# Performance work log

Hardware: AMD Instinct MI355X
Metric: run time of the kernel (lower is better)

Reference implementation:

```python
import jax, jax.numpy as jnp
import numpy as np

D1 = 2  # Predictor d1
D2 = 3  # Predictor d2


def setup_inputs() -> dict:
    key = jax.random.key(0)
    ks = jax.random.split(key, 8)
    B, S, W = 256, 16, 32
    V, E, H, C = 30000, 256, 512, 5
    abstracts = jax.random.randint(ks[0], (B, S, W), 0, V, dtype=jnp.int32)
    emb_table = jax.random.normal(ks[1], (V, E), dtype=jnp.float32) * 0.1
    # torch LSTMCell params: weight_ih [4H,E], weight_hh [4H,H], biases [4H]
    sc = 1.0 / np.sqrt(H)
    Wih = jax.random.uniform(ks[2], (4 * H, E), jnp.float32, -sc, sc)
    Whh = jax.random.uniform(ks[3], (4 * H, H), jnp.float32, -sc, sc)
    b_ih = jax.random.uniform(ks[4], (4 * H,), jnp.float32, -sc, sc)
    b_hh = jax.random.uniform(ks[5], (4 * H,), jnp.float32, -sc, sc)
    # Predictor: d1+1 weights [H,C], d2+1 weights [C,C], zero biases [1,C]
    W1 = jax.random.normal(ks[6], (D1 + 1, H, C), dtype=jnp.float32)
    W2 = jax.random.normal(ks[7], (D2 + 1, C, C), dtype=jnp.float32)
    b1 = jnp.zeros((1, C), dtype=jnp.float32)
    b2 = jnp.zeros((1, C), dtype=jnp.float32)
    return {"abstracts": abstracts, "emb_table": emb_table, "Wih": Wih,
            "Whh": Whh, "b_ih": b_ih, "b_hh": b_hh,
            "W1": W1, "b1": b1, "W2": W2, "b2": b2}


def _lstm_scan(x_tbe, Wih, Whh, b_ih, b_hh):
    # x_tbe: [T, B, E] time-major; state carried across ALL timesteps
    T, B, _ = x_tbe.shape
    H = Whh.shape[1]
    bias = b_ih + b_hh

    def step(carry, x):
        h, c = carry
        gates = x @ Wih.T + h @ Whh.T + bias  # [B, 4H]
        i_, f_, g_, o_ = jnp.split(gates, 4, axis=-1)
        c2 = jax.nn.sigmoid(f_) * c + jax.nn.sigmoid(i_) * jnp.tanh(g_)
        h2 = jax.nn.sigmoid(o_) * jnp.tanh(c2)
        return (h2, c2), h2

    init = (jnp.zeros((B, H), x_tbe.dtype), jnp.zeros((B, H), x_tbe.dtype))
    _, hs = jax.lax.scan(step, init, x_tbe)  # [T, B, H]
    return hs


def _predictor(reps, W1, b1, W2, b2):
    # reps: [S, B, H] sentence representations
    S = reps.shape[0]
    C = W1.shape[-1]
    # A[m] = tanh(sum_{k<=min(m,d1)} reps[m-k] @ W1[k] + b1)
    P = jnp.einsum('sbh,khc->ksbc', reps, W1)  # [d1+1, S, B, C]
    A_pre = jnp.zeros(reps.shape[:2] + (C,), reps.dtype)
    for k in range(D1 + 1):
        A_pre = A_pre.at[k:].add(P[k][:S - k])
    A = jnp.tanh(A_pre + b1)  # [S, B, C]
    # main branch (i >= d2): pred_i = logsoftmax(sum_t A[i-d2+t] @ W2[t] + b2)
    Q = jnp.einsum('sbc,tcd->tsbd', A, W2)  # [d2+1, S, B, C]
    M = sum(Q[t][t:S - D2 + t] for t in range(D2 + 1)) + b2  # [S-d2, B, C]
    # fallback (i < d2): logsoftmax(tanh(reps[i] @ W1[0] + b1) @ W2[0] + b2)
    F = jnp.tanh(jnp.einsum('sbh,hc->sbc', reps[:D2], W1[0]) + b1) @ W2[0] + b2
    preds = jnp.concatenate([jax.nn.log_softmax(F, axis=-1),
                             jax.nn.log_softmax(M, axis=-1)], axis=0)
    return preds  # [S, B, C]


def reference(abstracts, emb_table, Wih, Whh, b_ih, b_hh, W1, b1, W2, b2):
    B, S, W = abstracts.shape
    H = Whh.shape[1]
    emb = emb_table[abstracts]                 # [B, S, W, E]
    emb = jnp.transpose(emb, (1, 2, 0, 3))     # [S, W, B, E]
    x = emb.reshape(S * W, B, emb.shape[-1])   # time-major over all words
    hs = _lstm_scan(x, Wih, Whh, b_ih, b_hh)   # [S*W, B, H]
    hs = hs.reshape(S, W, B, H)
    reps = jnp.max(hs, axis=1)                 # max-pool over words -> [S, B, H]
    # dropout is identity in eval mode
    preds = _predictor(reps, W1, b1, W2, b2)   # [S, B, C]
    return jnp.transpose(preds, (1, 2, 0))     # [B, C, S]
```

## Files before the change

kernel.cpp:

```cpp
#include <hip/hip_runtime.h>
#include <cstdint>
#include <cstddef>

typedef float    f32x4  __attribute__((ext_vector_type(4)));
typedef short    s16x8  __attribute__((ext_vector_type(8)));
typedef _Float16 f16x8  __attribute__((ext_vector_type(8)));
typedef uint16_t u16x4  __attribute__((ext_vector_type(4)));

#define D_B 256
#define D_S 16
#define D_W 32
#define D_T 512
#define D_V 30000
#define D_E 256
#define D_H 512
#define D_G 2048
#define D_C 5

constexpr size_t OFF_EG    = 0;
constexpr size_t OFF_EMB   = OFF_EG   + (size_t)D_V * D_G * 2;
constexpr size_t OFF_WIH   = OFF_EMB  + (size_t)D_V * D_E * 2;
constexpr size_t OFF_WHH   = OFF_WIH  + (size_t)D_G * D_E * 2;
constexpr size_t OFF_BIAS  = OFF_WHH  + (size_t)D_G * D_H * 2;
constexpr size_t OFF_HBUF  = OFF_BIAS + (size_t)D_G * 4;
constexpr size_t OFF_FLAGS = OFF_HBUF + (size_t)2 * D_B * D_H * 2;
constexpr size_t OFF_REPS  = OFF_FLAGS + (size_t)256 * 4;
constexpr size_t OFF_A     = OFF_REPS + (size_t)D_S * D_B * D_H * 4;
constexpr size_t OFF_A0    = OFF_A    + (size_t)D_S * D_B * D_C * 4;
constexpr size_t OFF_ABT   = OFF_A0   + (size_t)3 * D_B * D_C * 4;


__device__ __forceinline__ uint16_t f2h(float f) {
    _Float16 h = (_Float16)f;
    return __builtin_bit_cast(uint16_t, h);
}
__device__ __forceinline__ float sigm(float x)  { return 1.0f / (1.0f + __expf(-x)); }
__device__ __forceinline__ float tanh_fast(float x) { return 1.0f - 2.0f / (__expf(2.0f * x) + 1.0f); }

#define VWAIT(N) do { asm volatile("s_waitcnt vmcnt(" #N ")" ::: "memory"); \
                      __builtin_amdgcn_sched_barrier(0); } while (0)
#define SBAR()   __builtin_amdgcn_sched_barrier(0)

__device__ __forceinline__ int load_flag_llc(const int* p) {
    int v;
    asm volatile("global_load_dword %0, %1, off sc0 sc1\n\ts_waitcnt vmcnt(0)"
                 : "=v"(v) : "v"(p) : "memory");
    return v;
}
__device__ __forceinline__ void store_dword_llc(int* p, int v) {
    asm volatile("global_store_dword %0, %1, off sc0 sc1" :: "v"(p), "v"(v) : "memory");
}
__device__ __forceinline__ void store16_llc(void* p, f32x4 v) {
    asm volatile("global_store_dwordx4 %0, %1, off sc0 sc1" :: "v"(p), "v"(v) : "memory");
}
__device__ __forceinline__ void store_h_nowait(uint16_t* p, f16x8 v) {
    asm volatile("global_store_dwordx4 %0, %1, off sc0 sc1" :: "v"(p), "v"(v) : "memory");
}
__device__ __forceinline__ void issue_tok(const int* p, int& v) {
    asm volatile("global_load_dword %0, %1, off" : "=&v"(v) : "v"(p) : "memory");
}
__device__ __forceinline__ void issue_eg(const uint16_t* p, f16x8& a, f16x8& b2,
                                         f16x8& c, f16x8& d) {
    asm volatile(
        "global_load_dwordx4 %0, %4, off\n\t"
        "global_load_dwordx4 %1, %4, off offset:16\n\t"
        "global_load_dwordx4 %2, %4, off offset:32\n\t"
        "global_load_dwordx4 %3, %4, off offset:48"
        : "=&v"(a), "=&v"(b2), "=&v"(c), "=&v"(d)
        : "v"(p) : "memory");
}
__device__ __forceinline__ void issue_h8(const uint16_t* base, f16x8* A) {
    const uint16_t* base2 = base + 2048;
    asm volatile(
        "global_load_dwordx4 %0, %8, off sc0 sc1\n\t"
        "global_load_dwordx4 %1, %8, off offset:1024 sc0 sc1\n\t"
        "global_load_dwordx4 %2, %8, off offset:2048 sc0 sc1\n\t"
        "global_load_dwordx4 %3, %8, off offset:3072 sc0 sc1\n\t"
        "global_load_dwordx4 %4, %9, off sc0 sc1\n\t"
        "global_load_dwordx4 %5, %9, off offset:1024 sc0 sc1\n\t"
        "global_load_dwordx4 %6, %9, off offset:2048 sc0 sc1\n\t"
        "global_load_dwordx4 %7, %9, off offset:3072 sc0 sc1"
        : "=&v"(A[0]), "=&v"(A[1]), "=&v"(A[2]), "=&v"(A[3]),
          "=&v"(A[4]), "=&v"(A[5]), "=&v"(A[6]), "=&v"(A[7])
        : "v"(base), "v"(base2) : "memory");
}

__global__ __launch_bounds__(256) void prep_kernel(
    const int* __restrict__ abstracts,
    const float* __restrict__ emb, const float* __restrict__ Wih,
    const float* __restrict__ Whh, const float* __restrict__ bih,
    const float* __restrict__ bhh,
    uint16_t* __restrict__ embB, uint16_t* __restrict__ WihP,
    uint16_t* __restrict__ WhhP, float* __restrict__ biasP,
    uint16_t* __restrict__ hbuf0, int* __restrict__ flags,
    int* __restrict__ abT)
{
    const long NA = (long)D_V * D_E / 4;
    const long NB = (long)D_G * D_E / 4;
    const long NC = (long)D_G * D_H / 4;
    const long ND = D_G;
    const long NE = (long)D_B * D_H / 8;
    const long NF = 256;
    const long NG = (long)D_T * D_B;
    const long TOT = NA + NB + NC + ND + NE + NF + NG;
    long stride = (long)gridDim.x * blockDim.x;
    for (long i = (long)blockIdx.x * blockDim.x + threadIdx.x; i < TOT; i += stride) {
        if (i < NA) {
            f32x4 v = ((const f32x4*)emb)[i];
            u16x4 o = { f2h(v[0]), f2h(v[1]), f2h(v[2]), f2h(v[3]) };
            ((u16x4*)embB)[i] = o;
        } else if (i < NA + NB) {
            long j = i - NA; long flat = j * 4;
            int r = (int)(flat >> 8), e0 = (int)(flat & 255);
            int p = ((r & 511) << 2) | (r >> 9);
            f32x4 v = ((const f32x4*)Wih)[j];
            u16x4 o = { f2h(v[0]), f2h(v[1]), f2h(v[2]), f2h(v[3]) };
            *(u16x4*)(WihP + (size_t)p * D_E + e0) = o;
        } else if (i < NA + NB + NC) {
            long j = i - NA - NB; long flat = j * 4;
            int r = (int)(flat >> 9), k0 = (int)(flat & 511);
            int p = ((r & 511) << 2) | (r >> 9);
            f32x4 v = ((const f32x4*)Whh)[j];
            u16x4 o = { f2h(v[0]), f2h(v[1]), f2h(v[2]), f2h(v[3]) };
            *(u16x4*)(WhhP + (size_t)p * D_H + k0) = o;
        } else if (i < NA + NB + NC + ND) {
            int p = (int)(i - NA - NB - NC);
            int r = ((p & 3) << 9) | (p >> 2);
            biasP[p] = bih[r] + bhh[r];
        } else if (i < NA + NB + NC + ND + NE) {
            long j = i - NA - NB - NC - ND;
            f32x4 z = (f32x4)0.0f;
            store16_llc(hbuf0 + j * 8, z);
        } else if (i < NA + NB + NC + ND + NE + NF) {
            long j = i - NA - NB - NC - ND - NE;
            store_dword_llc(flags + j, 0);
        } else {
            long j = i - NA - NB - NC - ND - NE - NF;
            int t = (int)(j >> 8), b = (int)(j & 255);
            abT[(size_t)t * D_B + b] = abstracts[(size_t)b * D_T + t];
        }
    }
    asm volatile("s_waitcnt vmcnt(0)" ::: "memory");
}

__global__ __launch_bounds__(256) void egemm_kernel(
    const uint16_t* __restrict__ embB, const uint16_t* __restrict__ WihP,
    uint16_t* __restrict__ EG)
{
    int nt = blockIdx.x;
    int mt = blockIdx.y;
    int tid = threadIdx.x, lane = tid & 63, wv = tid >> 6;
    int v0 = mt * 128, n0 = nt * 128;
    __shared__ uint16_t As[128][40];
    __shared__ uint16_t Bs[128][40];
    f32x4 acc[4][4];
#pragma unroll
    for (int a = 0; a < 4; ++a)
#pragma unroll
        for (int bb = 0; bb < 4; ++bb) acc[a][bb] = (f32x4)0.0f;
    int wm = (wv >> 1) * 64, wn = (wv & 1) * 64;
    int row = tid >> 1, half = tid & 1;
    for (int kb = 0; kb < 8; ++kb) {
        int k0 = kb * 32;
        int vrow = v0 + row; if (vrow > D_V - 1) vrow = D_V - 1;
        const s16x8* pa = (const s16x8*)(embB + (size_t)vrow * D_E + k0 + half * 16);
        *(s16x8*)&As[row][half * 16]     = pa[0];
        *(s16x8*)&As[row][half * 16 + 8] = pa[1];
        const s16x8* pb = (const s16x8*)(WihP + (size_t)(n0 + row) * D_E + k0 + half * 16);
        *(s16x8*)&Bs[row][half * 16]     = pb[0];
        *(s16x8*)&Bs[row][half * 16 + 8] = pb[1];
        __syncthreads();
        int krow = (lane >> 4) * 8;
        f16x8 af[4], bfr[4];
#pragma unroll
        for (int i = 0; i < 4; ++i) af[i]  = *(const f16x8*)&As[wm + i * 16 + (lane & 15)][krow];
#pragma unroll
        for (int i = 0; i < 4; ++i) bfr[i] = *(const f16x8*)&Bs[wn + i * 16 + (lane & 15)][krow];
#pragma unroll
        for (int mi = 0; mi < 4; ++mi)
#pragma unroll
            for (int ni = 0; ni < 4; ++ni)
                acc[mi][ni] = __builtin_amdgcn_mfma_f32_16x16x32_f16(af[mi], bfr[ni], acc[mi][ni], 0, 0, 0);
        __syncthreads();
    }
#pragma unroll
    for (int mi = 0; mi < 4; ++mi) {
        int rbase = v0 + wm + mi * 16 + (lane >> 4) * 4;
#pragma unroll
        for (int ni = 0; ni < 4; ++ni) {
            int col = n0 + wn + ni * 16 + (lane & 15);
#pragma unroll
            for (int r = 0; r < 4; ++r) {
                int vr = rbase + r;
                if (vr < D_V) EG[(size_t)vr * D_G + col] = f2h(acc[mi][ni][r]);
            }
        }
    }
}

#define MFMA_HALF(Aar, MT, KH)                                                         \
    _Pragma("unroll")                                                                  \
    for (int ks = 0; ks < 8; ++ks) {                                                   \
        acc[MT][0] = __builtin_amdgcn_mfma_f32_16x16x32_f16(Aar[ks], bq[0][(KH)*8+ks], acc[MT][0], 0, 0, 0); \
        acc[MT][1] = __builtin_amdgcn_mfma_f32_16x16x32_f16(Aar[ks], bq[1][(KH)*8+ks], acc[MT][1], 0, 0, 0); \
    }

#define LSTM_PHASE(T, TOKC, TOKN)                                                      \
do {                                                                                   \
    int tnext = (T) + 1; if (tnext > D_T - 1) tnext = D_T - 1;                         \
    issue_tok(abT + (size_t)tnext * D_B + b, TOKN);                                    \
    f16x8 ec0, ec1, ec2, ec3;                                                          \
    issue_eg(EG + (size_t)(TOKC) * D_G + rg * 32, ec0, ec1, ec2, ec3);                 \
    if ((T) > 0) {                                                                     \
        const int tgt = 64 * (T);                                                      \
        int guard = 0;                                                                 \
        while (true) {                                                                 \
            int f = load_flag_llc(ctr);        \
            if (f >= tgt) break;                                                       \
            if (++guard > (1 << 20)) break;                                            \
            __builtin_amdgcn_s_sleep(1);                                               \
        }                                                                              \
    } else {                                                                           \
        VWAIT(0);                                                                      \
    }                                                                                  \
    SBAR();                                                                            \
    const uint16_t* cur = hbuf + (size_t)((T) & 1) * (D_B * D_H);                      \
    const uint16_t* hb = cur + (size_t)bg * 4 * 8192 + lane * 8;                       \
    f16x8 A0[8], A1[8], A2[8], A3[8];                                                  \
    issue_h8(hb,                 A0);                                      \
    issue_h8(hb + 4096,          A1);                                      \
    issue_h8(hb + 8192,          A2);                                      \
    issue_h8(hb + 12288,         A3);                                      \
    f32x4 acc[4][2];                                                                   \
    _Pragma("unroll")                                                                  \
    for (int m = 0; m < 4; ++m) { acc[m][0] = (f32x4)0.0f; acc[m][1] = (f32x4)0.0f; }  \
    VWAIT(24); MFMA_HALF(A0, 0, 0); SBAR();                                            \
    issue_h8(hb + 16384, A0);                                              \
    VWAIT(24); MFMA_HALF(A1, 0, 1); SBAR();                                            \
    issue_h8(hb + 20480, A1);                                              \
    VWAIT(24); MFMA_HALF(A2, 1, 0); SBAR();                                            \
    issue_h8(hb + 24576, A2);                                              \
    VWAIT(24); MFMA_HALF(A3, 1, 1); SBAR();                                            \
    issue_h8(hb + 28672, A3);                                              \
    VWAIT(24); MFMA_HALF(A0, 2, 0); SBAR();                                            \
    VWAIT(16); MFMA_HALF(A1, 2, 1); SBAR();                                            \
    VWAIT(8);  MFMA_HALF(A2, 3, 0); SBAR();                                            \
    VWAIT(0);  MFMA_HALF(A3, 3, 1); SBAR();                                            \
              \
    _Pragma("unroll")                                                                  \
    for (int mtt = 0; mtt < 4; ++mtt) {                                                \
        int br = mtt * 16 + (lane >> 4) * 4;                                           \
        _Pragma("unroll")                                                              \
        for (int nt2 = 0; nt2 < 2; ++nt2) {                                            \
            int n = nt2 * 16 + (lane & 15);                                            \
            _Pragma("unroll")                                                          \
            for (int r = 0; r < 4; ++r) gfull[br + r][n] = acc[mtt][nt2][r];           \
        }                                                                              \
    }                                                                                  \
                                                 \
    float ev[32];                                                                      \
    _Pragma("unroll")                                                                  \
    for (int i = 0; i < 8; ++i) { ev[i] = (float)ec0[i]; ev[8 + i] = (float)ec1[i];    \
                                  ev[16 + i] = (float)ec2[i]; ev[24 + i] = (float)ec3[i]; } \
    f16x8 vh;                                                                          \
    _Pragma("unroll")                                                                  \
    for (int j = 0; j < 8; ++j) {                                                      \
        float gi = gfull[lane][j * 4 + 0] + bias_s[j * 4 + 0] + ev[j * 4 + 0];         \
        float gf = gfull[lane][j * 4 + 1] + bias_s[j * 4 + 1] + ev[j * 4 + 1];         \
        float gg = gfull[lane][j * 4 + 2] + bias_s[j * 4 + 2] + ev[j * 4 + 2];         \
        float go = gfull[lane][j * 4 + 3] + bias_s[j * 4 + 3] + ev[j * 4 + 3];         \
        float c2 = sigm(gf) * creg[j] + sigm(gi) * tanh_fast(gg);                      \
        float h2 = sigm(go) * tanh_fast(c2);                                           \
        creg[j] = c2;                                                                  \
        float rm = fmaxf(rreg[j], h2);                                                 \
        if (((T) & 31) == 31) {                                                        \
            reps[(size_t)((T) >> 5) * (D_B * D_H) + (size_t)b * D_H + rg * 8 + j] = rm;\
            rm = -1e30f;                                                               \
        }                                                                              \
        rreg[j] = rm;                                                                  \
        vh[j] = (_Float16)h2;                                                          \
    }                                                                                  \
    uint16_t* nxt = hbuf + (size_t)(((T) + 1) & 1) * (D_B * D_H);                      \
    store_h_nowait(nxt + (size_t)U * 8, vh);                                           \
    VWAIT(0);                         \
    if (lane == 0) atomicAdd(ctr, 1);               \
} while (0)

__global__ __launch_bounds__(64, 1) void lstm_seq_kernel(
    const int* __restrict__ abT, const uint16_t* __restrict__ EG,
    const uint16_t* __restrict__ WhhP, const float* __restrict__ biasP,
    uint16_t* __restrict__ hbuf, int* __restrict__ flags,
    float* __restrict__ reps)
{
    const int bid = blockIdx.x;
    const int rg = bid & 63;
    const int bg = bid >> 6;
    const int lane = threadIdx.x;
    __shared__ float gfull[64][33];
    __shared__ float bias_s[32];

    if (lane < 32) bias_s[lane] = biasP[rg * 32 + lane];

    float creg[8], rreg[8];
#pragma unroll
    for (int j = 0; j < 8; ++j) { creg[j] = 0.0f; rreg[j] = -1e30f; }

    const uint16_t* Wp = WhhP + (size_t)rg * 32 * D_H;
    f16x8 bq[2][16];
#pragma unroll
    for (int nt = 0; nt < 2; ++nt)
#pragma unroll
        for (int ks = 0; ks < 16; ++ks)
            bq[nt][ks] = *(const f16x8*)(Wp + (size_t)(nt * 16 + (lane & 15)) * D_H + ks * 32 + ((lane >> 4) * 8));

    const int b = bg * 64 + lane;
    const int U = ((b >> 4) << 10) + ((rg >> 2) << 6) + ((rg & 3) << 4) + (b & 15);
    int* ctr = flags + bg * 32;

    int tok_a = abT[b];
    int tok_b;

    for (int t = 0; t < D_T; t += 2) {
        LSTM_PHASE(t,     tok_a, tok_b);
        LSTM_PHASE(t + 1, tok_b, tok_a);
    }
}

__global__ __launch_bounds__(256) void predA_kernel(
    const float* __restrict__ reps, const float* __restrict__ W1,
    const float* __restrict__ b1, float* __restrict__ A, float* __restrict__ A0)
{
    int gw = blockIdx.x * 4 + (threadIdx.x >> 6);
    int lane = threadIdx.x & 63;
    int s = gw >> 8, b = gw & 255;
    float accT[5] = {0, 0, 0, 0, 0};
    float acc0[5] = {0, 0, 0, 0, 0};
    for (int k = 0; k <= 2; ++k) {
        if (s - k < 0) break;
        const float* rp = reps + ((size_t)(s - k) * D_B + b) * D_H;
        const float* w  = W1 + (size_t)k * D_H * D_C;
        float part[5] = {0, 0, 0, 0, 0};
#pragma unroll
        for (int i = 0; i < 8; ++i) {
            int h = lane * 8 + i;
            float rv = rp[h];
#pragma unroll
            for (int c = 0; c < 5; ++c) part[c] += rv * w[h * 5 + c];
        }
#pragma unroll
        for (int c = 0; c < 5; ++c) { accT[c] += part[c]; if (k == 0) acc0[c] = part[c]; }
    }
#pragma unroll
    for (int m = 1; m < 64; m <<= 1)
#pragma unroll
        for (int c = 0; c < 5; ++c) {
            accT[c] += __shfl_xor(accT[c], m, 64);
            acc0[c] += __shfl_xor(acc0[c], m, 64);
        }
    if (lane == 0) {
#pragma unroll
        for (int c = 0; c < 5; ++c) A[((size_t)s * D_B + b) * D_C + c] = tanhf(accT[c] + b1[c]);
        if (s < 3)
#pragma unroll
            for (int c = 0; c < 5; ++c) A0[((size_t)s * D_B + b) * D_C + c] = tanhf(acc0[c] + b1[c]);
    }
}

__global__ __launch_bounds__(256) void predOut_kernel(
    const float* __restrict__ A, const float* __restrict__ A0,
    const float* __restrict__ W2, const float* __restrict__ b2,
    float* __restrict__ out)
{
    int g = blockIdx.x * 256 + threadIdx.x;
    int b = g >> 4, s = g & 15;
    float v[5];
#pragma unroll
    for (int d = 0; d < 5; ++d) v[d] = b2[d];
    if (s < 3) {
        const float* Ar = A0 + ((size_t)s * D_B + b) * D_C;
#pragma unroll
        for (int c = 0; c < 5; ++c) {
            float a = Ar[c];
#pragma unroll
            for (int d = 0; d < 5; ++d) v[d] += a * W2[c * 5 + d];
        }
    } else {
        int i = s - 3;
        for (int tt = 0; tt < 4; ++tt) {
            const float* Ar = A + ((size_t)(tt + i) * D_B + b) * D_C;
            const float* w  = W2 + tt * 25;
#pragma unroll
            for (int c = 0; c < 5; ++c) {
                float a = Ar[c];
#pragma unroll
                for (int d = 0; d < 5; ++d) v[d] += a * w[c * 5 + d];
            }
        }
    }
    float m = v[0];
#pragma unroll
    for (int d = 1; d < 5; ++d) m = fmaxf(m, v[d]);
    float ssum = 0.0f;
#pragma unroll
    for (int d = 0; d < 5; ++d) ssum += expf(v[d] - m);
    float l = logf(ssum);
#pragma unroll
    for (int d = 0; d < 5; ++d) out[(size_t)b * 80 + d * 16 + s] = v[d] - m - l;
}

extern "C" void kernel_launch(void* const* d_in, const int* in_sizes, int n_in,
                              void* d_out, int out_size, void* d_ws, size_t ws_size,
                              hipStream_t stream)
{
    const int*   abstracts = (const int*)  d_in[0];
    const float* emb  = (const float*)d_in[1];
    const float* Wih  = (const float*)d_in[2];
    const float* Whh  = (const float*)d_in[3];
    const float* bih  = (const float*)d_in[4];
    const float* bhh  = (const float*)d_in[5];
    const float* W1   = (const float*)d_in[6];
    const float* b1   = (const float*)d_in[7];
    const float* W2   = (const float*)d_in[8];
    const float* b2   = (const float*)d_in[9];
    float* out = (float*)d_out;

    char* ws = (char*)d_ws;
    uint16_t* EG    = (uint16_t*)(ws + OFF_EG);
    uint16_t* embB  = (uint16_t*)(ws + OFF_EMB);
    uint16_t* WihP  = (uint16_t*)(ws + OFF_WIH);
    uint16_t* WhhP  = (uint16_t*)(ws + OFF_WHH);
    float*    biasP = (float*)   (ws + OFF_BIAS);
    uint16_t* hbuf  = (uint16_t*)(ws + OFF_HBUF);
    int*      flags = (int*)     (ws + OFF_FLAGS);
    float*    reps  = (float*)   (ws + OFF_REPS);
    float*    Abuf  = (float*)   (ws + OFF_A);
    float*    A0buf = (float*)   (ws + OFF_A0);
    int*      abT   = (int*)     (ws + OFF_ABT);

    prep_kernel<<<dim3(2048), dim3(256), 0, stream>>>(abstracts, emb, Wih, Whh, bih, bhh,
                                                      embB, WihP, WhhP, biasP, hbuf, flags, abT);
    egemm_kernel<<<dim3(16, 235), dim3(256), 0, stream>>>(embB, WihP, EG);
    lstm_seq_kernel<<<dim3(256), dim3(64), 0, stream>>>(abT, EG, WhhP, biasP,
                                                        hbuf, flags, reps);
    predA_kernel<<<dim3(1024), dim3(256), 0, stream>>>(reps, W1, b1, Abuf, A0buf);
    predOut_kernel<<<dim3(16), dim3(256), 0, stream>>>(Abuf, A0buf, W2, b2, out);
}
```

Before: 2.688 ms.

## Share h-state loads across four waves via LDS staging in LSTM recurrence

```diff
diff --git a/kernel.cpp b/kernel.cpp
--- a/kernel.cpp
+++ b/kernel.cpp
@@ -69,20 +69,32 @@
         : "=&v"(a), "=&v"(b2), "=&v"(c), "=&v"(d)
         : "v"(p) : "memory");
 }
-__device__ __forceinline__ void issue_h8(const uint16_t* base, f16x8* A) {
-    const uint16_t* base2 = base + 2048;
+__device__ __forceinline__ void issue_h16s(const uint16_t* base, f16x8* A) {
+    const uint16_t* b1 = base + 2048;
+    const uint16_t* b2 = base + 4096;
+    const uint16_t* b3 = base + 6144;
     asm volatile(
-        "global_load_dwordx4 %0, %8, off sc0 sc1\n\t"
-        "global_load_dwordx4 %1, %8, off offset:1024 sc0 sc1\n\t"
-        "global_load_dwordx4 %2, %8, off offset:2048 sc0 sc1\n\t"
-        "global_load_dwordx4 %3, %8, off offset:3072 sc0 sc1\n\t"
-        "global_load_dwordx4 %4, %9, off sc0 sc1\n\t"
-        "global_load_dwordx4 %5, %9, off offset:1024 sc0 sc1\n\t"
-        "global_load_dwordx4 %6, %9, off offset:2048 sc0 sc1\n\t"
-        "global_load_dwordx4 %7, %9, off offset:3072 sc0 sc1"
+        "global_load_dwordx4 %0,  %16, off sc0 sc1\n\t"
+        "global_load_dwordx4 %1,  %16, off offset:1024 sc0 sc1\n\t"
+        "global_load_dwordx4 %2,  %16, off offset:2048 sc0 sc1\n\t"
+        "global_load_dwordx4 %3,  %16, off offset:3072 sc0 sc1\n\t"
+        "global_load_dwordx4 %4,  %17, off sc0 sc1\n\t"
+        "global_load_dwordx4 %5,  %17, off offset:1024 sc0 sc1\n\t"
+        "global_load_dwordx4 %6,  %17, off offset:2048 sc0 sc1\n\t"
+        "global_load_dwordx4 %7,  %17, off offset:3072 sc0 sc1\n\t"
+        "global_load_dwordx4 %8,  %18, off sc0 sc1\n\t"
+        "global_load_dwordx4 %9,  %18, off offset:1024 sc0 sc1\n\t"
+        "global_load_dwordx4 %10, %18, off offset:2048 sc0 sc1\n\t"
+        "global_load_dwordx4 %11, %18, off offset:3072 sc0 sc1\n\t"
+        "global_load_dwordx4 %12, %19, off sc0 sc1\n\t"
+        "global_load_dwordx4 %13, %19, off offset:1024 sc0 sc1\n\t"
+        "global_load_dwordx4 %14, %19, off offset:2048 sc0 sc1\n\t"
+        "global_load_dwordx4 %15, %19, off offset:3072 sc0 sc1"
         : "=&v"(A[0]), "=&v"(A[1]), "=&v"(A[2]), "=&v"(A[3]),
-          "=&v"(A[4]), "=&v"(A[5]), "=&v"(A[6]), "=&v"(A[7])
-        : "v"(base), "v"(base2) : "memory");
+          "=&v"(A[4]), "=&v"(A[5]), "=&v"(A[6]), "=&v"(A[7]),
+          "=&v"(A[8]), "=&v"(A[9]), "=&v"(A[10]), "=&v"(A[11]),
+          "=&v"(A[12]), "=&v"(A[13]), "=&v"(A[14]), "=&v"(A[15])
+        : "v"(base), "v"(b1), "v"(b2), "v"(b3) : "memory");
 }
 
 __global__ __launch_bounds__(256) void prep_kernel(
@@ -198,13 +210,6 @@
     }
 }
 
-#define MFMA_HALF(Aar, MT, KH)                                                         \
-    _Pragma("unroll")                                                                  \
-    for (int ks = 0; ks < 8; ++ks) {                                                   \
-        acc[MT][0] = __builtin_amdgcn_mfma_f32_16x16x32_f16(Aar[ks], bq[0][(KH)*8+ks], acc[MT][0], 0, 0, 0); \
-        acc[MT][1] = __builtin_amdgcn_mfma_f32_16x16x32_f16(Aar[ks], bq[1][(KH)*8+ks], acc[MT][1], 0, 0, 0); \
-    }
-
 #define LSTM_PHASE(T, TOKC, TOKN)                                                      \
 do {                                                                                   \
     int tnext = (T) + 1; if (tnext > D_T - 1) tnext = D_T - 1;                         \
@@ -224,29 +229,34 @@
         VWAIT(0);                                                                      \
     }                                                                                  \
     SBAR();                                                                            \
+                    \
     const uint16_t* cur = hbuf + (size_t)((T) & 1) * (D_B * D_H);                      \
-    const uint16_t* hb = cur + (size_t)bg * 4 * 8192 + lane * 8;                       \
-    f16x8 A0[8], A1[8], A2[8], A3[8];                                                  \
-    issue_h8(hb,                 A0);                                      \
-    issue_h8(hb + 4096,          A1);                                      \
-    issue_h8(hb + 8192,          A2);                                      \
-    issue_h8(hb + 12288,         A3);                                      \
+    const uint16_t* src = cur + (size_t)(bg * 4 + wv) * 8192 + lane * 8;               \
+    f16x8 sA[16];                                                                      \
+    issue_h16s(src, sA);                                                               \
+    VWAIT(8);                                                                          \
+    _Pragma("unroll")                                                                  \
+    for (int ks = 0; ks < 8; ++ks)                                                     \
+        *(f16x8*)&hstage[(wv * 16 + ks) * 512 + lane * 8] = sA[ks];                    \
+    VWAIT(0);                                                                          \
+    _Pragma("unroll")                                                                  \
+    for (int ks = 8; ks < 16; ++ks)                                                    \
+        *(f16x8*)&hstage[(wv * 16 + ks) * 512 + lane * 8] = sA[ks];                    \
+    __syncthreads();                                       \
     f32x4 acc[4][2];                                                                   \
     _Pragma("unroll")                                                                  \
     for (int m = 0; m < 4; ++m) { acc[m][0] = (f32x4)0.0f; acc[m][1] = (f32x4)0.0f; }  \
-    VWAIT(24); MFMA_HALF(A0, 0, 0); SBAR();                                            \
-    issue_h8(hb + 16384, A0);                                              \
-    VWAIT(24); MFMA_HALF(A1, 0, 1); SBAR();                                            \
-    issue_h8(hb + 20480, A1);                                              \
-    VWAIT(24); MFMA_HALF(A2, 1, 0); SBAR();                                            \
-    issue_h8(hb + 24576, A2);                                              \
-    VWAIT(24); MFMA_HALF(A3, 1, 1); SBAR();                                            \
-    issue_h8(hb + 28672, A3);                                              \
-    VWAIT(24); MFMA_HALF(A0, 2, 0); SBAR();                                            \
-    VWAIT(16); MFMA_HALF(A1, 2, 1); SBAR();                                            \
-    VWAIT(8);  MFMA_HALF(A2, 3, 0); SBAR();                                            \
-    VWAIT(0);  MFMA_HALF(A3, 3, 1); SBAR();                                            \
-              \
+    _Pragma("unroll")                                                                  \
+    for (int mtt = 0; mtt < 4; ++mtt) {                                                \
+        _Pragma("unroll")                                                              \
+        for (int ks = 0; ks < 16; ++ks) {                                              \
+            f16x8 a = *(const f16x8*)&hstage[(mtt * 16 + ks) * 512 + lane * 8];        \
+            acc[mtt][0] = __builtin_amdgcn_mfma_f32_16x16x32_f16(a, bq[0][ks], acc[mtt][0], 0, 0, 0); \
+            acc[mtt][1] = __builtin_amdgcn_mfma_f32_16x16x32_f16(a, bq[1][ks], acc[mtt][1], 0, 0, 0); \
+        }                                                                              \
+    }                                                                                  \
+    __syncthreads();              \
+                                 \
     _Pragma("unroll")                                                                  \
     for (int mtt = 0; mtt < 4; ++mtt) {                                                \
         int br = mtt * 16 + (lane >> 4) * 4;                                           \
@@ -254,7 +264,7 @@
         for (int nt2 = 0; nt2 < 2; ++nt2) {                                            \
             int n = nt2 * 16 + (lane & 15);                                            \
             _Pragma("unroll")                                                          \
-            for (int r = 0; r < 4; ++r) gfull[br + r][n] = acc[mtt][nt2][r];           \
+            for (int r = 0; r < 4; ++r) gfull[wv][br + r][n] = acc[mtt][nt2][r];       \
         }                                                                              \
     }                                                                                  \
                                                  \
@@ -265,10 +275,10 @@
     f16x8 vh;                                                                          \
     _Pragma("unroll")                                                                  \
     for (int j = 0; j < 8; ++j) {                                                      \
-        float gi = gfull[lane][j * 4 + 0] + bias_s[j * 4 + 0] + ev[j * 4 + 0];         \
-        float gf = gfull[lane][j * 4 + 1] + bias_s[j * 4 + 1] + ev[j * 4 + 1];         \
-        float gg = gfull[lane][j * 4 + 2] + bias_s[j * 4 + 2] + ev[j * 4 + 2];         \
-        float go = gfull[lane][j * 4 + 3] + bias_s[j * 4 + 3] + ev[j * 4 + 3];         \
+        float gi = gfull[wv][lane][j * 4 + 0] + bias_s[wv][j * 4 + 0] + ev[j * 4 + 0]; \
+        float gf = gfull[wv][lane][j * 4 + 1] + bias_s[wv][j * 4 + 1] + ev[j * 4 + 1]; \
+        float gg = gfull[wv][lane][j * 4 + 2] + bias_s[wv][j * 4 + 2] + ev[j * 4 + 2]; \
+        float go = gfull[wv][lane][j * 4 + 3] + bias_s[wv][j * 4 + 3] + ev[j * 4 + 3]; \
         float c2 = sigm(gf) * creg[j] + sigm(gi) * tanh_fast(gg);                      \
         float h2 = sigm(go) * tanh_fast(c2);                                           \
         creg[j] = c2;                                                                  \
@@ -286,20 +296,23 @@
     if (lane == 0) atomicAdd(ctr, 1);               \
 } while (0)
 
-__global__ __launch_bounds__(64, 1) void lstm_seq_kernel(
+__global__ __launch_bounds__(256, 1) void lstm_seq_kernel(
     const int* __restrict__ abT, const uint16_t* __restrict__ EG,
     const uint16_t* __restrict__ WhhP, const float* __restrict__ biasP,
     uint16_t* __restrict__ hbuf, int* __restrict__ flags,
     float* __restrict__ reps)
 {
     const int bid = blockIdx.x;
-    const int rg = bid & 63;
-    const int bg = bid >> 6;
-    const int lane = threadIdx.x;
-    __shared__ float gfull[64][33];
-    __shared__ float bias_s[32];
-
-    if (lane < 32) bias_s[lane] = biasP[rg * 32 + lane];
+    const int q  = bid & 15;
+    const int bg = bid >> 4;
+    const int tid = threadIdx.x, lane = tid & 63, wv = tid >> 6;
+    const int rg = q * 4 + wv;
+
+    __shared__ uint16_t hstage[32768];
+    __shared__ float gfull[4][64][33];
+    __shared__ float bias_s[4][32];
+
+    if (tid < 128) bias_s[tid >> 5][tid & 31] = biasP[(q * 4 + (tid >> 5)) * 32 + (tid & 31)];
 
     float creg[8], rreg[8];
 #pragma unroll
@@ -312,6 +325,7 @@
 #pragma unroll
         for (int ks = 0; ks < 16; ++ks)
             bq[nt][ks] = *(const f16x8*)(Wp + (size_t)(nt * 16 + (lane & 15)) * D_H + ks * 32 + ((lane >> 4) * 8));
+    __syncthreads();
 
     const int b = bg * 64 + lane;
     const int U = ((b >> 4) << 10) + ((rg >> 2) << 6) + ((rg & 3) << 4) + (b & 15);
@@ -440,7 +454,7 @@
     prep_kernel<<<dim3(2048), dim3(256), 0, stream>>>(abstracts, emb, Wih, Whh, bih, bhh,
                                                       embB, WihP, WhhP, biasP, hbuf, flags, abT);
     egemm_kernel<<<dim3(16, 235), dim3(256), 0, stream>>>(embB, WihP, EG);
-    lstm_seq_kernel<<<dim3(256), dim3(64), 0, stream>>>(abT, EG, WhhP, biasP,
+    lstm_seq_kernel<<<dim3(64), dim3(256), 0, stream>>>(abT, EG, WhhP, biasP,
                                                         hbuf, flags, reps);
     predA_kernel<<<dim3(1024), dim3(256), 0, stream>>>(reps, W1, b1, Abuf, A0buf);
     predOut_kernel<<<dim3(16), dim3(256), 0, stream>>>(Abuf, A0buf, W2, b2, out);
```

Result: slower. 3.499 ms (+30.2%).

## Split LSTM recurrence across twice as many blocks with 32-row batch groups

Applied to the files above, without the earlier changes.

```diff
diff --git a/kernel.cpp b/kernel.cpp
--- a/kernel.cpp
+++ b/kernel.cpp
@@ -225,30 +225,22 @@
     }                                                                                  \
     SBAR();                                                                            \
     const uint16_t* cur = hbuf + (size_t)((T) & 1) * (D_B * D_H);                      \
-    const uint16_t* hb = cur + (size_t)bg * 4 * 8192 + lane * 8;                       \
+    const uint16_t* hb = cur + (size_t)bg8 * 2 * 8192 + lane * 8;                      \
     f16x8 A0[8], A1[8], A2[8], A3[8];                                                  \
     issue_h8(hb,                 A0);                                      \
     issue_h8(hb + 4096,          A1);                                      \
     issue_h8(hb + 8192,          A2);                                      \
     issue_h8(hb + 12288,         A3);                                      \
-    f32x4 acc[4][2];                                                                   \
+    f32x4 acc[2][2];                                                                   \
     _Pragma("unroll")                                                                  \
-    for (int m = 0; m < 4; ++m) { acc[m][0] = (f32x4)0.0f; acc[m][1] = (f32x4)0.0f; }  \
+    for (int m = 0; m < 2; ++m) { acc[m][0] = (f32x4)0.0f; acc[m][1] = (f32x4)0.0f; }  \
     VWAIT(24); MFMA_HALF(A0, 0, 0); SBAR();                                            \
-    issue_h8(hb + 16384, A0);                                              \
-    VWAIT(24); MFMA_HALF(A1, 0, 1); SBAR();                                            \
-    issue_h8(hb + 20480, A1);                                              \
-    VWAIT(24); MFMA_HALF(A2, 1, 0); SBAR();                                            \
-    issue_h8(hb + 24576, A2);                                              \
-    VWAIT(24); MFMA_HALF(A3, 1, 1); SBAR();                                            \
-    issue_h8(hb + 28672, A3);                                              \
-    VWAIT(24); MFMA_HALF(A0, 2, 0); SBAR();                                            \
-    VWAIT(16); MFMA_HALF(A1, 2, 1); SBAR();                                            \
-    VWAIT(8);  MFMA_HALF(A2, 3, 0); SBAR();                                            \
-    VWAIT(0);  MFMA_HALF(A3, 3, 1); SBAR();                                            \
+    VWAIT(16); MFMA_HALF(A1, 0, 1); SBAR();                                            \
+    VWAIT(8);  MFMA_HALF(A2, 1, 0); SBAR();                                            \
+    VWAIT(0);  MFMA_HALF(A3, 1, 1); SBAR();                                            \
               \
     _Pragma("unroll")                                                                  \
-    for (int mtt = 0; mtt < 4; ++mtt) {                                                \
+    for (int mtt = 0; mtt < 2; ++mtt) {                                                \
         int br = mtt * 16 + (lane >> 4) * 4;                                           \
         _Pragma("unroll")                                                              \
         for (int nt2 = 0; nt2 < 2; ++nt2) {                                            \
@@ -257,7 +249,7 @@
             for (int r = 0; r < 4; ++r) gfull[br + r][n] = acc[mtt][nt2][r];           \
         }                                                                              \
     }                                                                                  \
-                                                 \
+               \
     float ev[32];                                                                      \
     _Pragma("unroll")                                                                  \
     for (int i = 0; i < 8; ++i) { ev[i] = (float)ec0[i]; ev[8 + i] = (float)ec1[i];    \
@@ -265,23 +257,24 @@
     f16x8 vh;                                                                          \
     _Pragma("unroll")                                                                  \
     for (int j = 0; j < 8; ++j) {                                                      \
-        float gi = gfull[lane][j * 4 + 0] + bias_s[j * 4 + 0] + ev[j * 4 + 0];         \
-        float gf = gfull[lane][j * 4 + 1] + bias_s[j * 4 + 1] + ev[j * 4 + 1];         \
-        float gg = gfull[lane][j * 4 + 2] + bias_s[j * 4 + 2] + ev[j * 4 + 2];         \
-        float go = gfull[lane][j * 4 + 3] + bias_s[j * 4 + 3] + ev[j * 4 + 3];         \
+        float gi = gfull[row][j * 4 + 0] + bias_s[j * 4 + 0] + ev[j * 4 + 0];          \
+        float gf = gfull[row][j * 4 + 1] + bias_s[j * 4 + 1] + ev[j * 4 + 1];          \
+        float gg = gfull[row][j * 4 + 2] + bias_s[j * 4 + 2] + ev[j * 4 + 2];          \
+        float go = gfull[row][j * 4 + 3] + bias_s[j * 4 + 3] + ev[j * 4 + 3];          \
         float c2 = sigm(gf) * creg[j] + sigm(gi) * tanh_fast(gg);                      \
         float h2 = sigm(go) * tanh_fast(c2);                                           \
         creg[j] = c2;                                                                  \
         float rm = fmaxf(rreg[j], h2);                                                 \
         if (((T) & 31) == 31) {                                                        \
-            reps[(size_t)((T) >> 5) * (D_B * D_H) + (size_t)b * D_H + rg * 8 + j] = rm;\
+            if (lane < 32)                                                             \
+                reps[(size_t)((T) >> 5) * (D_B * D_H) + (size_t)b * D_H + rg * 8 + j] = rm; \
             rm = -1e30f;                                                               \
         }                                                                              \
         rreg[j] = rm;                                                                  \
         vh[j] = (_Float16)h2;                                                          \
     }                                                                                  \
     uint16_t* nxt = hbuf + (size_t)(((T) + 1) & 1) * (D_B * D_H);                      \
-    store_h_nowait(nxt + (size_t)U * 8, vh);                                           \
+    if (lane < 32) store_h_nowait(nxt + (size_t)U * 8, vh);                            \
     VWAIT(0);                         \
     if (lane == 0) atomicAdd(ctr, 1);               \
 } while (0)
@@ -293,10 +286,11 @@
     float* __restrict__ reps)
 {
     const int bid = blockIdx.x;
-    const int rg = bid & 63;
-    const int bg = bid >> 6;
+    const int rg  = bid & 63;
+    const int bg8 = bid >> 6;
     const int lane = threadIdx.x;
-    __shared__ float gfull[64][33];
+    const int row  = lane & 31;
+    __shared__ float gfull[32][33];
     __shared__ float bias_s[32];
 
     if (lane < 32) bias_s[lane] = biasP[rg * 32 + lane];
@@ -313,9 +307,9 @@
         for (int ks = 0; ks < 16; ++ks)
             bq[nt][ks] = *(const f16x8*)(Wp + (size_t)(nt * 16 + (lane & 15)) * D_H + ks * 32 + ((lane >> 4) * 8));
 
-    const int b = bg * 64 + lane;
+    const int b = bg8 * 32 + row;
     const int U = ((b >> 4) << 10) + ((rg >> 2) << 6) + ((rg & 3) << 4) + (b & 15);
-    int* ctr = flags + bg * 32;
+    int* ctr = flags + bg8 * 32;
 
     int tok_a = abT[b];
     int tok_b;
@@ -440,7 +434,7 @@
     prep_kernel<<<dim3(2048), dim3(256), 0, stream>>>(abstracts, emb, Wih, Whh, bih, bhh,
                                                       embB, WihP, WhhP, biasP, hbuf, flags, abT);
     egemm_kernel<<<dim3(16, 235), dim3(256), 0, stream>>>(embB, WihP, EG);
-    lstm_seq_kernel<<<dim3(256), dim3(64), 0, stream>>>(abT, EG, WhhP, biasP,
+    lstm_seq_kernel<<<dim3(512), dim3(64), 0, stream>>>(abT, EG, WhhP, biasP,
                                                         hbuf, flags, reps);
     predA_kernel<<<dim3(1024), dim3(256), 0, stream>>>(reps, W1, b1, Abuf, A0buf);
     predOut_kernel<<<dim3(16), dim3(256), 0, stream>>>(Abuf, A0buf, W2, b2, out);
```

Result: slower. 3.468 ms (+29.0%).
